# Kernel optimization log

Measured on AMD Instinct MI355X. Metric: run time of the kernel, lower is better.

The kernel has to match this reference:

```python
import jax, jax.numpy as jnp
import numpy as np

KEY_SIZE = 256

def setup_inputs() -> dict:
    key = jax.random.key(0)
    ks = jax.random.split(key, 4)
    B, C, T, K, V = 4, 512, 4096, 256, 256
    s = 1.0 / np.sqrt(C)
    return {
        "x": jax.random.normal(ks[0], (B, C, T), dtype=jnp.float32),
        "Wq": jax.random.normal(ks[1], (C, K), dtype=jnp.float32) * s,
        "bq": jnp.zeros((K,), dtype=jnp.float32),
        "Wk": jax.random.normal(ks[2], (C, K), dtype=jnp.float32) * s,
        "bk": jnp.zeros((K,), dtype=jnp.float32),
        "Wv": jax.random.normal(ks[3], (C, V), dtype=jnp.float32) * s,
        "bv": jnp.zeros((V,), dtype=jnp.float32),
    }

def reference(x, Wq, bq, Wk, bk, Wv, bv):
    # x: (B, C, T) -> (B, T, C)
    B, C, T = x.shape
    x_bt = jnp.transpose(x, (0, 2, 1))
    q = x_bt @ Wq + bq            # (B, T, K)
    k = x_bt @ Wk + bk            # (B, T, K)
    v = x_bt @ Wv + bv            # (B, T, V)
    logits = jnp.einsum('btk,bsk->bts', q, k) / jnp.sqrt(jnp.float32(KEY_SIZE))
    causal = jnp.tril(jnp.ones((T, T), dtype=bool))  # keep lower-triangular incl diag
    logits = jnp.where(causal, logits, -jnp.inf)
    attn = jax.nn.softmax(logits, axis=-1)
    read = jnp.einsum('bts,bsv->btv', attn, v)        # (B, T, V)
    out = jnp.concatenate([x_bt, read], axis=-1)      # (B, T, C+V)
    return jnp.transpose(out, (0, 2, 1))              # (B, C+V, T)
```

## Files before the change

### kernel.cpp

```cpp
#include <hip/hip_runtime.h>
#include <stdint.h>

#define Bn 4
#define Cn 512
#define Tn 4096
#define Kn 256
#define Nall 768

typedef __attribute__((ext_vector_type(8))) short bf16x8;
typedef __attribute__((ext_vector_type(4))) float f32x4;

__device__ __forceinline__ unsigned short f2bf(float f) {
  union { float f; unsigned int u; } v; v.f = f;
  unsigned int r = v.u + 0x7fffu + ((v.u >> 16) & 1u);
  return (unsigned short)(r >> 16);
}

__device__ __forceinline__ void gload_lds16(const void* g, void* l) {
  auto gp = reinterpret_cast<const __attribute__((address_space(1))) unsigned int*>(
      reinterpret_cast<uintptr_t>(g));
  auto lp = reinterpret_cast<__attribute__((address_space(3))) unsigned int*>(
      static_cast<unsigned int>(reinterpret_cast<uintptr_t>(l)));
  __builtin_amdgcn_global_load_lds(gp, lp, 16, 0, 0);
}

__device__ __forceinline__ f32x4 mfma16(bf16x8 a, bf16x8 b, f32x4 c) {
  return __builtin_amdgcn_mfma_f32_16x16x32_bf16(a, b, c, 0, 0, 0);
}

__global__ __launch_bounds__(256) void prep_x_kernel(const float* __restrict__ x,
    float* __restrict__ out, unsigned short* __restrict__ xt) {
  const int tt = blockIdx.x, cc = blockIdx.y, b = blockIdx.z;
  __shared__ unsigned short tile[64][66];
  const int tid = threadIdx.x;
#pragma unroll
  for (int e = 0; e < 4; ++e) {
    int f = e * 256 + tid;
    int row = f >> 4, c4 = f & 15;
    size_t gi = ((size_t)(b * Cn + cc * 64 + row)) * Tn + tt * 64 + c4 * 4;
    float4 v = *(const float4*)(x + gi);
    size_t go = ((size_t)(b * Nall + cc * 64 + row)) * Tn + tt * 64 + c4 * 4;
    *(float4*)(out + go) = v;
    tile[row][c4 * 4 + 0] = f2bf(v.x);
    tile[row][c4 * 4 + 1] = f2bf(v.y);
    tile[row][c4 * 4 + 2] = f2bf(v.z);
    tile[row][c4 * 4 + 3] = f2bf(v.w);
  }
  __syncthreads();
#pragma unroll
  for (int e = 0; e < 2; ++e) {
    int f = e * 256 + tid;
    int trow = f >> 3, cv = f & 7;
    bf16x8 vv;
#pragma unroll
    for (int j = 0; j < 8; ++j) vv[j] = (short)tile[cv * 8 + j][trow];
    *(bf16x8*)(xt + ((size_t)(b * Tn) + tt * 64 + trow) * Cn + cc * 64 + cv * 8) = vv;
  }
}

__global__ __launch_bounds__(256) void prep_w_kernel(const float* __restrict__ Wq,
    const float* __restrict__ Wk, const float* __restrict__ Wv,
    const float* __restrict__ bq, const float* __restrict__ bk, const float* __restrict__ bv,
    unsigned short* __restrict__ wt, float* __restrict__ bias) {
  int idx = blockIdx.x * 256 + threadIdx.x;
  int n = idx >> 9, c = idx & 511;
  const float* W = (n < 256) ? Wq : ((n < 512) ? Wk : Wv);
  wt[idx] = f2bf(W[c * 256 + (n & 255)]);
  if (idx < Nall) {
    const float* bb = (idx < 256) ? bq : ((idx < 512) ? bk : bv);
    bias[idx] = bb[idx & 255];
  }
}

__global__ __launch_bounds__(256) void qkv_gemm_kernel(const unsigned short* __restrict__ xt,
    const unsigned short* __restrict__ wt, const float* __restrict__ bias,
    unsigned short* __restrict__ qb, unsigned short* __restrict__ kb,
    unsigned short* __restrict__ vt) {
  const int t0 = blockIdx.x * 128, n0 = blockIdx.y * 128, b = blockIdx.z;
  __shared__ char at[8192];
  __shared__ char bt[8192];
  const int tid = threadIdx.x, w = tid >> 6, lane = tid & 63, g = lane >> 4, lr = lane & 15;
  const int wm = w >> 1, wn = w & 1;
  f32x4 acc[4][4];
#pragma unroll
  for (int i = 0; i < 4; ++i)
#pragma unroll
    for (int j = 0; j < 4; ++j) acc[i][j] = (f32x4){0.f, 0.f, 0.f, 0.f};

  const unsigned short* xtp = xt + ((size_t)b * Tn + t0) * Cn;
  for (int c0 = 0; c0 < Cn; c0 += 32) {
    __syncthreads();
#pragma unroll
    for (int i = 0; i < 2; ++i) {
      int off = i * 4096 + w * 1024 + lane * 16;
      int row = off >> 6, col = off & 63;
      gload_lds16(xtp + (size_t)row * Cn + c0 + (col >> 1), at + i * 4096 + w * 1024);
      gload_lds16(wt + (size_t)(n0 + row) * Cn + c0 + (col >> 1), bt + i * 4096 + w * 1024);
    }
    __syncthreads();
    bf16x8 af[4], bfr[4];
#pragma unroll
    for (int mt = 0; mt < 4; ++mt)
      af[mt] = *(const bf16x8*)(at + (wm * 64 + mt * 16 + lr) * 64 + g * 16);
#pragma unroll
    for (int nt = 0; nt < 4; ++nt)
      bfr[nt] = *(const bf16x8*)(bt + (wn * 64 + nt * 16 + lr) * 64 + g * 16);
#pragma unroll
    for (int mt = 0; mt < 4; ++mt)
#pragma unroll
      for (int nt = 0; nt < 4; ++nt)
        acc[mt][nt] = mfma16(af[mt], bfr[nt], acc[mt][nt]);
  }
#pragma unroll
  for (int nt = 0; nt < 4; ++nt) {
    int n = n0 + wn * 64 + nt * 16 + lr;
    float bval = bias[n];
#pragma unroll
    for (int mt = 0; mt < 4; ++mt) {
#pragma unroll
      for (int r = 0; r < 4; ++r) {
        int t = t0 + wm * 64 + mt * 16 + g * 4 + r;
        unsigned short h = f2bf(acc[mt][nt][r] + bval);
        if (n < 256) {
          qb[((size_t)(b * Tn) + t) * Kn + n] = h;
        } else if (n < 512) {
          int nc = n - 256;
          kb[((size_t)(b * Tn) + t) * Kn + (nc ^ ((t & 7) << 3))] = h;
        } else {
          int vc = n - 512;
          int tl = t & 63;
          vt[((size_t)(b * Kn) + vc) * Tn + (t & ~63) + (tl ^ ((vc & 7) << 3))] = h;
        }
      }
    }
  }
}

__global__ __launch_bounds__(256) void attn_kernel(const unsigned short* __restrict__ qb,
    const unsigned short* __restrict__ kb, const unsigned short* __restrict__ vt,
    float* __restrict__ out) {
  const int tile = blockIdx.x, b = blockIdx.y;
  const int qt0 = tile * 64;
  __shared__ char kbuf[32768];
  __shared__ char vbuf[32768];
  const int tid = threadIdx.x, w = tid >> 6, lane = tid & 63, g = lane >> 4, lr = lane & 15;
  const float SCL = 0.09016844005555521f;

  const unsigned short* qrow = qb + ((size_t)(b * Tn) + qt0 + w * 16 + lr) * Kn;
  bf16x8 qf[8];
#pragma unroll
  for (int kc = 0; kc < 8; ++kc) qf[kc] = *(const bf16x8*)(qrow + kc * 32 + g * 8);

  f32x4 o[16];
#pragma unroll
  for (int nt = 0; nt < 16; ++nt) o[nt] = (f32x4){0.f, 0.f, 0.f, 0.f};
  float m2[4], lsum[4];
#pragma unroll
  for (int r = 0; r < 4; ++r) { m2[r] = -1e30f; lsum[r] = 0.f; }

  const unsigned short* kbp = kb + (size_t)(b * Tn) * Kn;
  const unsigned short* vtp = vt + (size_t)(b * Kn) * Tn;
  const int nsteps = tile + 1;

  for (int s = 0; s < nsteps; ++s) {
    const int s0 = s * 64;
    __syncthreads();
#pragma unroll
    for (int i = 0; i < 8; ++i) {
      int off = i * 4096 + w * 1024 + lane * 16;
      { int row = off >> 9, col = off & 511;
        gload_lds16(kbp + (size_t)(s0 + row) * Kn + (col >> 1), kbuf + i * 4096 + w * 1024); }
      { int row = off >> 7, col = off & 127;
        gload_lds16(vtp + (size_t)row * Tn + s0 + (col >> 1), vbuf + i * 4096 + w * 1024); }
    }
    __syncthreads();

    f32x4 sfr[4];
#pragma unroll
    for (int ct = 0; ct < 4; ++ct) sfr[ct] = (f32x4){0.f, 0.f, 0.f, 0.f};
#pragma unroll
    for (int kc = 0; kc < 8; ++kc) {
#pragma unroll
      for (int ct = 0; ct < 4; ++ct) {
        int srow = ct * 16 + lr;
        bf16x8 kf = *(const bf16x8*)(kbuf + srow * 512 +
                                     ((kc * 64 + g * 16) ^ ((srow & 7) << 4)));
        sfr[ct] = mfma16(qf[kc], kf, sfr[ct]);
      }
    }

    float sv[4][4];
    const bool diag = (s0 == qt0);
#pragma unroll
    for (int ct = 0; ct < 4; ++ct)
#pragma unroll
      for (int r = 0; r < 4; ++r) {
        float v = sfr[ct][r] * SCL;
        if (diag) {
          int trow = qt0 + w * 16 + g * 4 + r;
          int scol = s0 + ct * 16 + lr;
          if (scol > trow) v = -1e30f;
        }
        sv[ct][r] = v;
      }
    float mt_[4];
#pragma unroll
    for (int r = 0; r < 4; ++r)
      mt_[r] = fmaxf(fmaxf(sv[0][r], sv[1][r]), fmaxf(sv[2][r], sv[3][r]));
#pragma unroll
    for (int d = 1; d < 16; d <<= 1)
#pragma unroll
      for (int r = 0; r < 4; ++r)
        mt_[r] = fmaxf(mt_[r], __shfl_xor(mt_[r], d, 64));
    float al[4], rs[4];
#pragma unroll
    for (int r = 0; r < 4; ++r) {
      float mn = fmaxf(m2[r], mt_[r]);
      al[r] = __builtin_amdgcn_exp2f(m2[r] - mn);
      m2[r] = mn;
      rs[r] = 0.f;
    }
    unsigned short ph[4][4];
#pragma unroll
    for (int ct = 0; ct < 4; ++ct)
#pragma unroll
      for (int r = 0; r < 4; ++r) {
        float p = __builtin_amdgcn_exp2f(sv[ct][r] - m2[r]);
        rs[r] += p;
        ph[ct][r] = f2bf(p);
      }
#pragma unroll
    for (int d = 1; d < 16; d <<= 1)
#pragma unroll
      for (int r = 0; r < 4; ++r)
        rs[r] += __shfl_xor(rs[r], d, 64);
#pragma unroll
    for (int r = 0; r < 4; ++r) lsum[r] = lsum[r] * al[r] + rs[r];
#pragma unroll
    for (int nt = 0; nt < 16; ++nt)
#pragma unroll
      for (int r = 0; r < 4; ++r) o[nt][r] *= al[r];

    __syncthreads();
    char* pbw = kbuf + w * 2048;
#pragma unroll
    for (int ct = 0; ct < 4; ++ct)
#pragma unroll
      for (int r = 0; r < 4; ++r) {
        int row = g * 4 + r;
        int colb = (ct * 16 + lr) * 2;
        *(unsigned short*)(pbw + row * 128 + (colb ^ ((row & 7) << 4))) = ph[ct][r];
      }
    bf16x8 pa[2];
#pragma unroll
    for (int kc2 = 0; kc2 < 2; ++kc2)
      pa[kc2] = *(const bf16x8*)(pbw + lr * 128 +
                                 ((kc2 * 64 + g * 16) ^ ((lr & 7) << 4)));
#pragma unroll
    for (int nt = 0; nt < 16; ++nt) {
      int vrow = nt * 16 + lr;
#pragma unroll
      for (int kc2 = 0; kc2 < 2; ++kc2) {
        bf16x8 vf = *(const bf16x8*)(vbuf + vrow * 128 +
                                     ((kc2 * 64 + g * 16) ^ ((vrow & 7) << 4)));
        o[nt] = mfma16(pa[kc2], vf, o[nt]);
      }
    }
  }

  float inv[4];
#pragma unroll
  for (int r = 0; r < 4; ++r) inv[r] = 1.0f / lsum[r];
  float* outp = out + ((size_t)(b * Nall) + 512) * Tn;
#pragma unroll
  for (int nt = 0; nt < 16; ++nt) {
#pragma unroll
    for (int r = 0; r < 4; ++r) {
      int n = nt * 16 + lr;
      int t = qt0 + w * 16 + g * 4 + r;
      outp[(size_t)n * Tn + t] = o[nt][r] * inv[r];
    }
  }
}

extern "C" void kernel_launch(void* const* d_in, const int* in_sizes, int n_in,
                              void* d_out, int out_size, void* d_ws, size_t ws_size,
                              hipStream_t stream) {
  const float* x  = (const float*)d_in[0];
  const float* Wq = (const float*)d_in[1];
  const float* bq = (const float*)d_in[2];
  const float* Wk = (const float*)d_in[3];
  const float* bk = (const float*)d_in[4];
  const float* Wv = (const float*)d_in[5];
  const float* bv = (const float*)d_in[6];
  float* out = (float*)d_out;
  char* ws = (char*)d_ws;

  unsigned short* xt = (unsigned short*)(ws);
  unsigned short* wt = (unsigned short*)(ws + 16777216);
  float*        bias = (float*)(ws + 17563648);
  unsigned short* qb = (unsigned short*)(ws + 17566720);
  unsigned short* kb = (unsigned short*)(ws + 25955328);
  unsigned short* vt = (unsigned short*)(ws + 34343936);

  prep_w_kernel<<<1536, 256, 0, stream>>>(Wq, Wk, Wv, bq, bk, bv, wt, bias);
  prep_x_kernel<<<dim3(64, 8, 4), 256, 0, stream>>>(x, out, xt);
  qkv_gemm_kernel<<<dim3(32, 6, 4), 256, 0, stream>>>(xt, wt, bias, qb, kb, vt);
  attn_kernel<<<dim3(64, 4), 256, 0, stream>>>(qb, kb, vt, out);
}
```

Baseline: 320.2 us.

## Split long causal attention rows into KV chunks with a separate merge kernel

The attention grid becomes 640 work items. Query tiles beyond the 16th have their KV range split into chunks of 16 steps, and each chunk writes unnormalized partial outputs plus max and sum to workspace. A new merge kernel combines these partials with log-sum-exp weighting for the later tiles, while early tiles still write directly. This targets load imbalance and the long tail from the causal triangle on 256 CUs. It adds an extra launch, partial-output traffic through global memory, and a dedicated P buffer in LDS, which also removes one barrier.

```diff
diff --git a/kernel.cpp b/kernel.cpp
--- a/kernel.cpp
+++ b/kernel.cpp
@@ -138,11 +138,25 @@
 
 __global__ __launch_bounds__(256) void attn_kernel(const unsigned short* __restrict__ qb,
     const unsigned short* __restrict__ kb, const unsigned short* __restrict__ vt,
-    float* __restrict__ out) {
-  const int tile = blockIdx.x, b = blockIdx.y;
-  const int qt0 = tile * 64;
+    float* __restrict__ po, float* __restrict__ ml, float* __restrict__ out) {
+  const int wg = blockIdx.x;
+  const int b = (wg >> 1) & 3;
+  const int item = ((wg >> 3) << 1) | (wg & 1);
+  int i = item, t = 0, c = 0, pre16 = 0;
+  for (t = 0; t < 64; ++t) {
+    int cnt = (t >> 4) + 1;
+    if (i < cnt) { c = i; break; }
+    i -= cnt;
+    if (t >= 16) pre16 += cnt;
+  }
+  const bool direct = (t < 16);
+  const int slot = b * 144 + pre16 + c;
+  const int qt0 = t * 64;
+  const int sb = c * 16, se = min(sb + 16, t + 1);
+
   __shared__ char kbuf[32768];
   __shared__ char vbuf[32768];
+  __shared__ char pbuf[8192];
   const int tid = threadIdx.x, w = tid >> 6, lane = tid & 63, g = lane >> 4, lr = lane & 15;
   const float SCL = 0.09016844005555521f;
 
@@ -160,18 +174,18 @@
 
   const unsigned short* kbp = kb + (size_t)(b * Tn) * Kn;
   const unsigned short* vtp = vt + (size_t)(b * Kn) * Tn;
-  const int nsteps = tile + 1;
-
-  for (int s = 0; s < nsteps; ++s) {
+  char* pbw = pbuf + w * 2048;
+
+  for (int s = sb; s < se; ++s) {
     const int s0 = s * 64;
     __syncthreads();
 #pragma unroll
-    for (int i = 0; i < 8; ++i) {
-      int off = i * 4096 + w * 1024 + lane * 16;
+    for (int i2 = 0; i2 < 8; ++i2) {
+      int off = i2 * 4096 + w * 1024 + lane * 16;
       { int row = off >> 9, col = off & 511;
-        gload_lds16(kbp + (size_t)(s0 + row) * Kn + (col >> 1), kbuf + i * 4096 + w * 1024); }
+        gload_lds16(kbp + (size_t)(s0 + row) * Kn + (col >> 1), kbuf + i2 * 4096 + w * 1024); }
       { int row = off >> 7, col = off & 127;
-        gload_lds16(vtp + (size_t)row * Tn + s0 + (col >> 1), vbuf + i * 4096 + w * 1024); }
+        gload_lds16(vtp + (size_t)row * Tn + s0 + (col >> 1), vbuf + i2 * 4096 + w * 1024); }
     }
     __syncthreads();
 
@@ -241,8 +255,6 @@
 #pragma unroll
       for (int r = 0; r < 4; ++r) o[nt][r] *= al[r];
 
-    __syncthreads();
-    char* pbw = kbuf + w * 2048;
 #pragma unroll
     for (int ct = 0; ct < 4; ++ct)
 #pragma unroll
@@ -268,18 +280,59 @@
     }
   }
 
-  float inv[4];
-#pragma unroll
-  for (int r = 0; r < 4; ++r) inv[r] = 1.0f / lsum[r];
-  float* outp = out + ((size_t)(b * Nall) + 512) * Tn;
-#pragma unroll
-  for (int nt = 0; nt < 16; ++nt) {
-#pragma unroll
-    for (int r = 0; r < 4; ++r) {
-      int n = nt * 16 + lr;
-      int t = qt0 + w * 16 + g * 4 + r;
-      outp[(size_t)n * Tn + t] = o[nt][r] * inv[r];
-    }
+  if (direct) {
+    float inv[4];
+#pragma unroll
+    for (int r = 0; r < 4; ++r) inv[r] = 1.0f / lsum[r];
+    float* outp = out + ((size_t)(b * Nall) + 512) * Tn;
+#pragma unroll
+    for (int nt = 0; nt < 16; ++nt)
+#pragma unroll
+      for (int r = 0; r < 4; ++r)
+        outp[(size_t)(nt * 16 + lr) * Tn + qt0 + w * 16 + g * 4 + r] = o[nt][r] * inv[r];
+  } else {
+    float* pob = po + (size_t)slot * 16384;
+#pragma unroll
+    for (int nt = 0; nt < 16; ++nt)
+#pragma unroll
+      for (int r = 0; r < 4; ++r)
+        pob[(w * 16 + g * 4 + r) * 256 + nt * 16 + lr] = o[nt][r];
+    if (lr == 0) {
+#pragma unroll
+      for (int r = 0; r < 4; ++r) {
+        ml[(size_t)slot * 128 + w * 16 + g * 4 + r] = m2[r];
+        ml[(size_t)slot * 128 + 64 + w * 16 + g * 4 + r] = lsum[r];
+      }
+    }
+  }
+}
+
+__global__ __launch_bounds__(256) void merge_kernel(const float* __restrict__ po,
+    const float* __restrict__ ml, float* __restrict__ out) {
+  const int t = blockIdx.x + 16, b = blockIdx.y, n = threadIdx.x;
+  const int nc = (t >> 4) + 1;
+  int pre16 = 0;
+  for (int u = 16; u < t; ++u) pre16 += (u >> 4) + 1;
+  const int slot0 = b * 144 + pre16;
+
+  float* outp = out + ((size_t)(b * Nall + 512) + n) * Tn + t * 64;
+  for (int r4 = 0; r4 < 16; ++r4) {
+    float4 vv;
+#pragma unroll
+    for (int j = 0; j < 4; ++j) {
+      int r = r4 * 4 + j;
+      float M = -1e30f;
+      for (int cc = 0; cc < nc; ++cc)
+        M = fmaxf(M, ml[(size_t)(slot0 + cc) * 128 + r]);
+      float L = 0.f, val = 0.f;
+      for (int cc = 0; cc < nc; ++cc) {
+        float mw = __builtin_amdgcn_exp2f(ml[(size_t)(slot0 + cc) * 128 + r] - M);
+        L += ml[(size_t)(slot0 + cc) * 128 + 64 + r] * mw;
+        val += po[(size_t)(slot0 + cc) * 16384 + r * 256 + n] * mw;
+      }
+      vv[j] = val / L;
+    }
+    *(float4*)(outp + r4 * 4) = vv;
   }
 }
 
@@ -296,15 +349,18 @@
   float* out = (float*)d_out;
   char* ws = (char*)d_ws;
 
-  unsigned short* xt = (unsigned short*)(ws);
-  unsigned short* wt = (unsigned short*)(ws + 16777216);
-  float*        bias = (float*)(ws + 17563648);
-  unsigned short* qb = (unsigned short*)(ws + 17566720);
-  unsigned short* kb = (unsigned short*)(ws + 25955328);
-  unsigned short* vt = (unsigned short*)(ws + 34343936);
+  unsigned short* qb = (unsigned short*)(ws);
+  unsigned short* kb = (unsigned short*)(ws + 8388608);
+  unsigned short* vt = (unsigned short*)(ws + 16777216);
+  unsigned short* xt = (unsigned short*)(ws + 25165824);
+  unsigned short* wt = (unsigned short*)(ws + 41943040);
+  float*        bias = (float*)(ws + 42729472);
+  float*          po = (float*)(ws + 25165824);
+  float*          mlb = (float*)(ws + 62914560);
 
   prep_w_kernel<<<1536, 256, 0, stream>>>(Wq, Wk, Wv, bq, bk, bv, wt, bias);
   prep_x_kernel<<<dim3(64, 8, 4), 256, 0, stream>>>(x, out, xt);
   qkv_gemm_kernel<<<dim3(32, 6, 4), 256, 0, stream>>>(xt, wt, bias, qb, kb, vt);
-  attn_kernel<<<dim3(64, 4), 256, 0, stream>>>(qb, kb, vt, out);
-}
+  attn_kernel<<<640, 256, 0, stream>>>(qb, kb, vt, po, mlb, out);
+  merge_kernel<<<dim3(48, 4), 256, 0, stream>>>(po, mlb, out);
+}
```

New measurement: 356.9 us. +11.5%, slower.
